# Performance work log

Measured on AMD Instinct MI355X. Metric: run time of the kernel, lower is better.

The kernel has to match this reference:

```python
import jax, jax.numpy as jnp
import numpy as np

B, LQ, LK = 4, 2048, 2048
DQ = DK = DV = DH = 1024


def _xavier(key, shape):
    fan_out, fan_in = shape
    bound = float(np.sqrt(6.0 / (fan_in + fan_out)))
    return jax.random.uniform(key, shape, jnp.float32, -bound, bound)


def setup_inputs() -> dict:
    key = jax.random.key(0)
    ks = jax.random.split(key, 6)
    query = jax.random.normal(ks[0], (B, LQ, DQ), jnp.float32)
    k_in = jax.random.normal(ks[1], (B, LK, DK), jnp.float32)
    key_mask = jax.random.randint(ks[2], (B, LK), 0, 2).astype(bool)
    # torch nn.Linear weights are [out_features, in_features]
    Wk = _xavier(ks[3], (2 * DH, DK))
    bk = jnp.zeros((2 * DH,), jnp.float32)
    Wq = _xavier(ks[4], (DH, DQ))
    bq = jnp.zeros((DH,), jnp.float32)
    Wfc = _xavier(ks[5], (DV, DH))
    bfc = jnp.zeros((DV,), jnp.float32)
    return {"query": query, "key": k_in, "key_mask": key_mask,
            "Wq": Wq, "bq": bq, "Wk": Wk, "bk": bk, "Wfc": Wfc, "bfc": bfc}


def reference(query, key, key_mask, Wq, bq, Wk, bk, Wfc, bfc):
    bs, timesteps, _ = key.shape
    dim = DH
    q = query @ Wq.T + bq                       # [B, Lq, dim]
    c = (key @ Wk.T + bk).reshape(bs, timesteps, 2, dim)
    k = c[:, :, 0]                              # [B, Lk, dim]
    v = c[:, :, 1]                              # [B, Lk, dim]
    scores = jnp.einsum('bqd,bkd->bqk', q, k)   # [B, Lq, Lk]
    scores = jnp.where(key_mask[:, None, :], -jnp.inf, scores)
    attn = jax.nn.softmax(scores, axis=-1)
    out = jnp.einsum('bqk,bkd->bqd', attn, v)   # [B, Lq, dim]
    out = out @ Wfc.T + bfc                     # [B, Lq, DV] (dropout p=0 / eval)
    return out
```

## Files before the change

### kernel.cpp

```cpp
#include <hip/hip_runtime.h>

typedef __attribute__((ext_vector_type(8))) _Float16 half8;
typedef __attribute__((ext_vector_type(4))) _Float16 half4;
typedef __attribute__((ext_vector_type(4))) float f32x4;

__global__ __launch_bounds__(256) void conv4_k(const float4* __restrict__ in,
                                               half4* __restrict__ out){
  int i = blockIdx.x * 256 + threadIdx.x;
  float4 v = in[i];
  half4 h = { (_Float16)v.x, (_Float16)v.y, (_Float16)v.z, (_Float16)v.w };
  out[i] = h;
}

__global__ void mask_detect(const unsigned int* __restrict__ m, int* __restrict__ flag){
  if (threadIdx.x == 0 && blockIdx.x == 0){
    int ok = 1;
#pragma unroll
    for (int j = 0; j < 16; j++){
      unsigned v = m[j];
      if (v != 0u && v != 1u && v != 0x3f800000u) ok = 0;
    }
    *flag = ok;
  }
}

__global__ __launch_bounds__(256) void softmax2048(const float* __restrict__ S,
                                                   _Float16* __restrict__ P){
  const long row = blockIdx.x;
  const float* s = S + row * 2048;
  _Float16* p = P + row * 2048;
  const int tid = threadIdx.x;
  float v[8];
  float m = -1e30f;
#pragma unroll
  for (int i = 0; i < 8; i++){ v[i] = s[tid + i * 256]; m = fmaxf(m, v[i]); }
#pragma unroll
  for (int o = 32; o; o >>= 1) m = fmaxf(m, __shfl_xor(m, o));
  __shared__ float rm[4], rs[4];
  if ((tid & 63) == 0) rm[tid >> 6] = m;
  __syncthreads();
  m = fmaxf(fmaxf(rm[0], rm[1]), fmaxf(rm[2], rm[3]));
  float sum = 0.f;
#pragma unroll
  for (int i = 0; i < 8; i++){ v[i] = __expf(v[i] - m); sum += v[i]; }
#pragma unroll
  for (int o = 32; o; o >>= 1) sum += __shfl_xor(sum, o);
  if ((tid & 63) == 0) rs[tid >> 6] = sum;
  __syncthreads();
  sum = rs[0] + rs[1] + rs[2] + rs[3];
  const float inv = 1.0f / sum;
#pragma unroll
  for (int i = 0; i < 8; i++) p[tid + i * 256] = (_Float16)(v[i] * inv);
}

#define GLL(gp, ldsoff) \
  __builtin_amdgcn_global_load_lds((const __attribute__((address_space(1))) void*)(gp), \
                                   (__attribute__((address_space(3))) void*)&lds[ldsoff], 16, 0, 0)

template<int EPI>
__global__ __launch_bounds__(256)
void gemm_bt(const unsigned short* __restrict__ A, const unsigned short* __restrict__ B,
             int lda, int ldb, int K,
             const float* __restrict__ bias, const void* __restrict__ mask,
             const int* __restrict__ maskFlag,
             void* __restrict__ out0, int ldc,
             long aBS, long bBS, long oBS, int maskBS)
{
  __shared__ short lds[2 * 128 * 32];

  const int z = blockIdx.z;
  const long zA = (long)z * aBS, zB = (long)z * bBS;
  const int tid = threadIdx.x;
  const int lane = tid & 63, wid = tid >> 6;
  const int wr = wid >> 1, wc = wid & 1;
  const int fr = lane & 15, fk = lane >> 4;
  const int brow = blockIdx.x * 128, bcol = blockIdx.y * 128;

  f32x4 acc[4][4];
  const f32x4 fzero = {0.f, 0.f, 0.f, 0.f};
#pragma unroll
  for (int i = 0; i < 4; i++)
#pragma unroll
    for (int j = 0; j < 4; j++) acc[i][j] = fzero;

  const int offA = (wr * 64 + fr) * 32 + fk * 8;
  const int offB = (wc * 64 + fr) * 32 + fk * 8;
  const int srow = tid >> 2;
  const int sck  = (tid & 3) * 8;

  for (int k0 = 0; k0 < K; k0 += 32) {
    __syncthreads();
    {
      const unsigned short* gA = A + zA + (long)(brow + srow) * lda + k0 + sck;
      GLL(gA, tid * 8);
      GLL(gA + (long)64 * lda, (256 + tid) * 8);
      const unsigned short* gB = B + zB + (long)(bcol + srow) * ldb + k0 + sck;
      GLL(gB, 4096 + tid * 8);
      GLL(gB + (long)64 * ldb, 4096 + (256 + tid) * 8);
    }
    __syncthreads();

    half8 a[4], b[4];
#pragma unroll
    for (int i = 0; i < 4; i++){
      a[i] = *(const half8*)&lds[offA + i * 512];
      b[i] = *(const half8*)&lds[4096 + offB + i * 512];
    }
#pragma unroll
    for (int mi = 0; mi < 4; mi++)
#pragma unroll
      for (int ni = 0; ni < 4; ni++)
        acc[mi][ni] = __builtin_amdgcn_mfma_f32_16x16x32_f16(a[mi], b[ni], acc[mi][ni], 0, 0, 0);
  }

  const long zO = (long)z * oBS;
  int mflag = 0;
  if constexpr (EPI == 1) mflag = *maskFlag;
#pragma unroll
  for (int mi = 0; mi < 4; mi++){
#pragma unroll
    for (int ni = 0; ni < 4; ni++){
      const int col = bcol + wc * 64 + ni * 16 + fr;
      float bv = 0.f;
      if constexpr (EPI != 1) { if (bias) bv = bias[col]; }
      bool msk = false;
      if constexpr (EPI == 1) {
        msk = mflag ? (((const int*)mask)[(long)z * maskBS + col] != 0)
                    : (((const unsigned char*)mask)[(long)z * maskBS + col] != 0);
      }
#pragma unroll
      for (int r = 0; r < 4; r++){
        const int row = brow + wr * 64 + mi * 16 + fk * 4 + r;
        float v = acc[mi][ni][r] + bv;
        if constexpr (EPI == 0) {
          ((float*)out0)[zO + (long)row * ldc + col] = v;
        } else if constexpr (EPI == 1) {
          ((float*)out0)[zO + (long)row * ldc + col] = msk ? -1e30f : v;
        } else if constexpr (EPI == 2) {
          ((_Float16*)out0)[zO + (long)row * ldc + col] = (_Float16)v;
        } else {
          const int bb = row >> 11, t = row & 2047;
          ((_Float16*)out0)[(long)bb * 2048 * 1024 + (long)col * 2048 + t] = (_Float16)v;
        }
      }
    }
  }
}

extern "C" void kernel_launch(void* const* d_in, const int* in_sizes, int n_in,
                              void* d_out, int out_size, void* d_ws, size_t ws_size,
                              hipStream_t stream)
{
  (void)in_sizes; (void)n_in; (void)out_size; (void)ws_size;
  const float* query = (const float*)d_in[0];
  const float* key   = (const float*)d_in[1];
  const void*  kmask = d_in[2];
  const float* Wq    = (const float*)d_in[3];
  const float* bq    = (const float*)d_in[4];
  const float* Wk    = (const float*)d_in[5];
  const float* bk    = (const float*)d_in[6];
  const float* Wfc   = (const float*)d_in[7];
  const float* bfc   = (const float*)d_in[8];
  float* out = (float*)d_out;

  char* ws = (char*)d_ws;
  size_t o = 0;
  auto take = [&](size_t bytes)->char*{
    char* p = ws + o;
    o += (bytes + 255) & ~(size_t)255;
    return p;
  };
  const size_t SZ_H = (size_t)8192 * 1024 * 2;

  int* maskFlag           = (int*)take(256);
  unsigned short* query_h = (unsigned short*)take(SZ_H);
  unsigned short* key_h   = (unsigned short*)take(SZ_H);
  unsigned short* Wq_h    = (unsigned short*)take((size_t)1024 * 1024 * 2);
  unsigned short* Wk_h    = (unsigned short*)take((size_t)2048 * 1024 * 2);
  unsigned short* Wfc_h   = (unsigned short*)take((size_t)1024 * 1024 * 2);
  unsigned short* Q       = (unsigned short*)take(SZ_H);
  unsigned short* K       = (unsigned short*)take(SZ_H);
  unsigned short* VT      = (unsigned short*)take(SZ_H);
  unsigned short* O       = (unsigned short*)take(SZ_H);
  float*          S       = (float*)take((size_t)8192 * 2048 * 4);
  unsigned short* P       = (unsigned short*)take((size_t)8192 * 2048 * 2);

  mask_detect<<<1, 64, 0, stream>>>((const unsigned int*)kmask, maskFlag);

  conv4_k<<<8192, 256, 0, stream>>>((const float4*)query, (half4*)query_h);
  conv4_k<<<8192, 256, 0, stream>>>((const float4*)key,   (half4*)key_h);
  conv4_k<<<1024, 256, 0, stream>>>((const float4*)Wq,    (half4*)Wq_h);
  conv4_k<<<2048, 256, 0, stream>>>((const float4*)Wk,    (half4*)Wk_h);
  conv4_k<<<1024, 256, 0, stream>>>((const float4*)Wfc,   (half4*)Wfc_h);

  gemm_bt<2><<<dim3(64, 8, 1), 256, 0, stream>>>(
      query_h, Wq_h, 1024, 1024, 1024,
      bq, nullptr, nullptr, Q, 1024, 0, 0, 0, 0);

  gemm_bt<2><<<dim3(64, 8, 1), 256, 0, stream>>>(
      key_h, Wk_h, 1024, 1024, 1024,
      bk, nullptr, nullptr, K, 1024, 0, 0, 0, 0);

  gemm_bt<4><<<dim3(64, 8, 1), 256, 0, stream>>>(
      key_h, Wk_h + (size_t)1024 * 1024, 1024, 1024, 1024,
      bk + 1024, nullptr, nullptr, VT, 0, 0, 0, 0, 0);

  gemm_bt<1><<<dim3(16, 16, 4), 256, 0, stream>>>(
      Q, K, 1024, 1024, 1024,
      nullptr, kmask, maskFlag, S, 2048,
      (long)2048 * 1024, (long)2048 * 1024, (long)2048 * 2048, 2048);

  softmax2048<<<8192, 256, 0, stream>>>(S, (_Float16*)P);

  gemm_bt<2><<<dim3(16, 8, 4), 256, 0, stream>>>(
      P, VT, 2048, 2048, 2048,
      nullptr, nullptr, nullptr, O, 1024,
      (long)2048 * 2048, (long)1024 * 2048, (long)2048 * 1024, 0);

  gemm_bt<0><<<dim3(64, 8, 1), 256, 0, stream>>>(
      O, Wfc_h, 1024, 1024, 1024,
      bfc, nullptr, nullptr, out, 1024, 0, 0, 0, 0);
}
```

Baseline: 403.2 us.

## Double-buffer LDS tiles in gemm_bt to overlap global loads with MFMA

The GEMM main loop now uses two LDS buffers. It issues the asynchronous global-to-LDS loads for the next K tile before running the MFMAs on the current tile, and needs only one barrier per iteration instead of two. The goal is to hide global memory latency behind matrix-core work in every GEMM stage of the attention pipeline. In exchange, LDS use per block doubles to 32 KB, which may reduce occupancy. Correctness relies on the barrier waiting for the outstanding global_load_lds transfers.

```diff
diff --git a/kernel.cpp b/kernel.cpp
--- a/kernel.cpp
+++ b/kernel.cpp
@@ -66,7 +66,7 @@
              void* __restrict__ out0, int ldc,
              long aBS, long bBS, long oBS, int maskBS)
 {
-  __shared__ short lds[2 * 128 * 32];
+  __shared__ short lds[2 * 8192];
 
   const int z = blockIdx.z;
   const long zA = (long)z * aBS, zB = (long)z * bBS;
@@ -88,30 +88,43 @@
   const int srow = tid >> 2;
   const int sck  = (tid & 3) * 8;
 
-  for (int k0 = 0; k0 < K; k0 += 32) {
-    __syncthreads();
-    {
-      const unsigned short* gA = A + zA + (long)(brow + srow) * lda + k0 + sck;
-      GLL(gA, tid * 8);
-      GLL(gA + (long)64 * lda, (256 + tid) * 8);
-      const unsigned short* gB = B + zB + (long)(bcol + srow) * ldb + k0 + sck;
-      GLL(gB, 4096 + tid * 8);
-      GLL(gB + (long)64 * ldb, 4096 + (256 + tid) * 8);
-    }
-    __syncthreads();
-
+  const unsigned short* gA0 = A + zA + (long)(brow + srow) * lda + sck;
+  const unsigned short* gB0 = B + zB + (long)(bcol + srow) * ldb + sck;
+  const long a64 = (long)64 * lda, b64 = (long)64 * ldb;
+
+#define STAGE(base, k0)                              \
+  do {                                               \
+    GLL(gA0 + (k0),       (base) + tid * 8);         \
+    GLL(gA0 + (k0) + a64, (base) + (256 + tid) * 8); \
+    GLL(gB0 + (k0),       (base) + 4096 + tid * 8);  \
+    GLL(gB0 + (k0) + b64, (base) + 4096 + (256 + tid) * 8); \
+  } while (0)
+
+  const int nt = K >> 5;
+  STAGE(0, 0);
+  __syncthreads();
+
+  int cur = 0;
+  for (int t = 0; t < nt; ++t) {
+    if (t + 1 < nt) STAGE((cur ^ 1) * 8192, (t + 1) << 5);
+
+    const int ab = cur * 8192;
     half8 a[4], b[4];
 #pragma unroll
     for (int i = 0; i < 4; i++){
-      a[i] = *(const half8*)&lds[offA + i * 512];
-      b[i] = *(const half8*)&lds[4096 + offB + i * 512];
+      a[i] = *(const half8*)&lds[ab + offA + i * 512];
+      b[i] = *(const half8*)&lds[ab + 4096 + offB + i * 512];
     }
 #pragma unroll
     for (int mi = 0; mi < 4; mi++)
 #pragma unroll
       for (int ni = 0; ni < 4; ni++)
         acc[mi][ni] = __builtin_amdgcn_mfma_f32_16x16x32_f16(a[mi], b[ni], acc[mi][ni], 0, 0, 0);
+
+    __syncthreads();
+    cur ^= 1;
   }
+#undef STAGE
 
   const long zO = (long)z * oBS;
   int mflag = 0;
```

Result: faster. 362.0 us (-10.2%).

## Replace GEMM with 256-row double-buffered pipelined kernel using 512 threads

Applied to the files above, without the earlier changes.

Replaces the 128x128, 256-thread, single-buffered GEMM with a 256xBN tile (BN=128 or 256), 512-thread kernel. The new kernel double-buffers LDS with a K-step of 64 and splits each iteration into phases so async global-to-LDS loads for the next tile overlap with MFMA work, using raw barriers, vmcnt waits and setprio. The aim is to hide load latency and raise data reuse per LDS byte. The cost is more LDS and registers per block, and fewer blocks on the smaller GEMMs, which lowers grid parallelism.

```diff
diff --git a/kernel.cpp b/kernel.cpp
--- a/kernel.cpp
+++ b/kernel.cpp
@@ -56,71 +56,130 @@
 #define GLL(gp, ldsoff) \
   __builtin_amdgcn_global_load_lds((const __attribute__((address_space(1))) void*)(gp), \
                                    (__attribute__((address_space(3))) void*)&lds[ldsoff], 16, 0, 0)
-
-template<int EPI>
-__global__ __launch_bounds__(256)
-void gemm_bt(const unsigned short* __restrict__ A, const unsigned short* __restrict__ B,
-             int lda, int ldb, int K,
-             const float* __restrict__ bias, const void* __restrict__ mask,
-             const int* __restrict__ maskFlag,
-             void* __restrict__ out0, int ldc,
-             long aBS, long bBS, long oBS, int maskBS)
+#define BAR() asm volatile("s_barrier" ::: "memory")
+#define VMCNT(n) asm volatile("s_waitcnt vmcnt(" #n ")" ::: "memory")
+
+template<int EPI, int NREP>
+__global__ __launch_bounds__(512, 2)
+void gemm256(const unsigned short* __restrict__ A, const unsigned short* __restrict__ B,
+             int lda, int ldb, int K, const float* __restrict__ bias,
+             const void* __restrict__ mask, const int* __restrict__ maskFlag,
+             void* __restrict__ out0, int ldc, long aBS, long bBS, long oBS, int maskBS)
 {
-  __shared__ short lds[2 * 128 * 32];
+  constexpr int BN     = 64 * NREP;
+  constexpr int BUFSZ  = 16384 + 4096 * NREP;
+  constexpr int NCHUNK = 2 + NREP / 2;
+  __shared__ short lds[2 * BUFSZ];
 
   const int z = blockIdx.z;
   const long zA = (long)z * aBS, zB = (long)z * bBS;
   const int tid = threadIdx.x;
   const int lane = tid & 63, wid = tid >> 6;
-  const int wr = wid >> 1, wc = wid & 1;
+  const int wr = wid >> 2, wc = wid & 3;
   const int fr = lane & 15, fk = lane >> 4;
-  const int brow = blockIdx.x * 128, bcol = blockIdx.y * 128;
-
-  f32x4 acc[4][4];
+  const int brow = blockIdx.x * 256, bcol = blockIdx.y * BN;
+
+  f32x4 acc[8][NREP];
   const f32x4 fzero = {0.f, 0.f, 0.f, 0.f};
 #pragma unroll
-  for (int i = 0; i < 4; i++)
-#pragma unroll
-    for (int j = 0; j < 4; j++) acc[i][j] = fzero;
-
-  const int offA = (wr * 64 + fr) * 32 + fk * 8;
-  const int offB = (wc * 64 + fr) * 32 + fk * 8;
-  const int srow = tid >> 2;
-  const int sck  = (tid & 3) * 8;
-
-  for (int k0 = 0; k0 < K; k0 += 32) {
-    __syncthreads();
-    {
-      const unsigned short* gA = A + zA + (long)(brow + srow) * lda + k0 + sck;
-      GLL(gA, tid * 8);
-      GLL(gA + (long)64 * lda, (256 + tid) * 8);
-      const unsigned short* gB = B + zB + (long)(bcol + srow) * ldb + k0 + sck;
-      GLL(gB, 4096 + tid * 8);
-      GLL(gB + (long)64 * ldb, 4096 + (256 + tid) * 8);
-    }
-    __syncthreads();
-
-    half8 a[4], b[4];
-#pragma unroll
-    for (int i = 0; i < 4; i++){
-      a[i] = *(const half8*)&lds[offA + i * 512];
-      b[i] = *(const half8*)&lds[4096 + offB + i * 512];
-    }
-#pragma unroll
-    for (int mi = 0; mi < 4; mi++)
-#pragma unroll
-      for (int ni = 0; ni < 4; ni++)
-        acc[mi][ni] = __builtin_amdgcn_mfma_f32_16x16x32_f16(a[mi], b[ni], acc[mi][ni], 0, 0, 0);
+  for (int i = 0; i < 8; i++)
+#pragma unroll
+    for (int j = 0; j < NREP; j++) acc[i][j] = fzero;
+
+  const int srow = tid >> 3, scol = (tid & 7) * 8;
+  const unsigned short* Ag = A + zA + (long)(brow + srow) * lda + scol;
+  const unsigned short* Bg = B + zB + (long)(bcol + srow) * ldb + scol;
+  const int aoff = (wr * 128 + fr) * 64 + fk * 8;
+  const int boff = (wc * 16 * NREP + fr) * 64 + fk * 8;
+
+  auto stage = [&](int nb, int c, long k1) {
+    if (c < 2) {
+      const unsigned short* g = Ag + (long)(c * 128) * lda + k1;
+      GLL(g,                  nb + c * 8192 + tid * 8);
+      GLL(g + (long)64 * lda, nb + c * 8192 + 4096 + tid * 8);
+    } else {
+      const unsigned short* g = Bg + (long)((c - 2) * 128) * ldb + k1;
+      GLL(g,                  nb + 16384 + (c - 2) * 8192 + tid * 8);
+      GLL(g + (long)64 * ldb, nb + 16384 + (c - 2) * 8192 + 4096 + tid * 8);
+    }
+  };
+
+  half8 a[4][2], b[NREP][2];
+  auto readA = [&](int cb, int qm) {
+#pragma unroll
+    for (int mi = 0; mi < 4; ++mi)
+#pragma unroll
+      for (int kk = 0; kk < 2; ++kk)
+        a[mi][kk] = *(const half8*)&lds[cb + aoff + qm * 4096 + mi * 1024 + kk * 32];
+  };
+  auto readB = [&](int cb, int n0, int n1) {
+#pragma unroll
+    for (int ni = n0; ni < n1; ++ni)
+#pragma unroll
+      for (int kk = 0; kk < 2; ++kk)
+        b[ni][kk] = *(const half8*)&lds[cb + 16384 + boff + ni * 1024 + kk * 32];
+  };
+  auto mmaQ = [&](int qm, int n0, int n1) {
+#pragma unroll
+    for (int mi = 0; mi < 4; ++mi)
+#pragma unroll
+      for (int ni = n0; ni < n1; ++ni) {
+        f32x4 c = acc[qm * 4 + mi][ni];
+        c = __builtin_amdgcn_mfma_f32_16x16x32_f16(a[mi][0], b[ni][0], c, 0, 0, 0);
+        c = __builtin_amdgcn_mfma_f32_16x16x32_f16(a[mi][1], b[ni][1], c, 0, 0, 0);
+        acc[qm * 4 + mi][ni] = c;
+      }
+  };
+
+  const int nt = K >> 6;
+  for (int c = 0; c < NCHUNK; ++c) stage(0, c, 0);
+
+  for (int t = 0; t < nt; ++t) {
+    const int cb = (t & 1) ? BUFSZ : 0, nb = cb ^ BUFSZ;
+    const long k1 = (long)(t + 1) << 6;
+    const bool pf = (t + 1 < nt);
+    if constexpr (NREP == 4) {
+      if (pf) { stage(nb, 0, k1); VMCNT(2); } else VMCNT(0);
+      BAR();
+      readA(cb, 0); readB(cb, 0, 2);
+      __builtin_amdgcn_s_setprio(1); mmaQ(0, 0, 2); __builtin_amdgcn_s_setprio(0);
+      BAR();
+      if (pf) stage(nb, 1, k1);
+      readB(cb, 2, 4);
+      BAR();
+      __builtin_amdgcn_s_setprio(1); mmaQ(0, 2, 4); __builtin_amdgcn_s_setprio(0);
+      BAR();
+      if (pf) stage(nb, 2, k1);
+      readA(cb, 1);
+      BAR();
+      __builtin_amdgcn_s_setprio(1); mmaQ(1, 2, 4); __builtin_amdgcn_s_setprio(0);
+      BAR();
+      if (pf) stage(nb, 3, k1);
+      BAR();
+      __builtin_amdgcn_s_setprio(1); mmaQ(1, 0, 2); __builtin_amdgcn_s_setprio(0);
+      BAR();
+    } else {
+      if (pf) { stage(nb, 0, k1); stage(nb, 1, k1); VMCNT(4); } else VMCNT(0);
+      BAR();
+      readA(cb, 0); readB(cb, 0, 2);
+      __builtin_amdgcn_s_setprio(1); mmaQ(0, 0, 2); __builtin_amdgcn_s_setprio(0);
+      BAR();
+      if (pf) stage(nb, 2, k1);
+      readA(cb, 1);
+      BAR();
+      __builtin_amdgcn_s_setprio(1); mmaQ(1, 0, 2); __builtin_amdgcn_s_setprio(0);
+      BAR();
+    }
   }
 
   const long zO = (long)z * oBS;
   int mflag = 0;
   if constexpr (EPI == 1) mflag = *maskFlag;
 #pragma unroll
-  for (int mi = 0; mi < 4; mi++){
-#pragma unroll
-    for (int ni = 0; ni < 4; ni++){
-      const int col = bcol + wc * 64 + ni * 16 + fr;
+  for (int mi = 0; mi < 8; ++mi) {
+#pragma unroll
+    for (int ni = 0; ni < NREP; ++ni) {
+      const int col = bcol + wc * 16 * NREP + ni * 16 + fr;
       float bv = 0.f;
       if constexpr (EPI != 1) { if (bias) bv = bias[col]; }
       bool msk = false;
@@ -129,8 +188,8 @@
                     : (((const unsigned char*)mask)[(long)z * maskBS + col] != 0);
       }
 #pragma unroll
-      for (int r = 0; r < 4; r++){
-        const int row = brow + wr * 64 + mi * 16 + fk * 4 + r;
+      for (int r = 0; r < 4; ++r) {
+        const int row = brow + wr * 128 + mi * 16 + fk * 4 + r;
         float v = acc[mi][ni][r] + bv;
         if constexpr (EPI == 0) {
           ((float*)out0)[zO + (long)row * ldc + col] = v;
@@ -139,8 +198,8 @@
         } else if constexpr (EPI == 2) {
           ((_Float16*)out0)[zO + (long)row * ldc + col] = (_Float16)v;
         } else {
-          const int bb = row >> 11, t = row & 2047;
-          ((_Float16*)out0)[(long)bb * 2048 * 1024 + (long)col * 2048 + t] = (_Float16)v;
+          const int bb = row >> 11, tt = row & 2047;
+          ((_Float16*)out0)[(long)bb * 2048 * 1024 + (long)col * 2048 + tt] = (_Float16)v;
         }
       }
     }
@@ -193,31 +252,31 @@
   conv4_k<<<2048, 256, 0, stream>>>((const float4*)Wk,    (half4*)Wk_h);
   conv4_k<<<1024, 256, 0, stream>>>((const float4*)Wfc,   (half4*)Wfc_h);
 
-  gemm_bt<2><<<dim3(64, 8, 1), 256, 0, stream>>>(
+  gemm256<2, 2><<<dim3(32, 8, 1), 512, 0, stream>>>(
       query_h, Wq_h, 1024, 1024, 1024,
       bq, nullptr, nullptr, Q, 1024, 0, 0, 0, 0);
 
-  gemm_bt<2><<<dim3(64, 8, 1), 256, 0, stream>>>(
+  gemm256<2, 2><<<dim3(32, 8, 1), 512, 0, stream>>>(
       key_h, Wk_h, 1024, 1024, 1024,
       bk, nullptr, nullptr, K, 1024, 0, 0, 0, 0);
 
-  gemm_bt<4><<<dim3(64, 8, 1), 256, 0, stream>>>(
+  gemm256<4, 2><<<dim3(32, 8, 1), 512, 0, stream>>>(
       key_h, Wk_h + (size_t)1024 * 1024, 1024, 1024, 1024,
       bk + 1024, nullptr, nullptr, VT, 0, 0, 0, 0, 0);
 
-  gemm_bt<1><<<dim3(16, 16, 4), 256, 0, stream>>>(
+  gemm256<1, 4><<<dim3(8, 8, 4), 512, 0, stream>>>(
       Q, K, 1024, 1024, 1024,
       nullptr, kmask, maskFlag, S, 2048,
       (long)2048 * 1024, (long)2048 * 1024, (long)2048 * 2048, 2048);
 
   softmax2048<<<8192, 256, 0, stream>>>(S, (_Float16*)P);
 
-  gemm_bt<2><<<dim3(16, 8, 4), 256, 0, stream>>>(
+  gemm256<2, 2><<<dim3(8, 8, 4), 512, 0, stream>>>(
       P, VT, 2048, 2048, 2048,
       nullptr, nullptr, nullptr, O, 1024,
       (long)2048 * 2048, (long)1024 * 2048, (long)2048 * 1024, 0);
 
-  gemm_bt<0><<<dim3(64, 8, 1), 256, 0, stream>>>(
+  gemm256<0, 2><<<dim3(32, 8, 1), 512, 0, stream>>>(
       O, Wfc_h, 1024, 1024, 1024,
       bfc, nullptr, nullptr, out, 1024, 0, 0, 0, 0);
 }
```

New measurement: 406.1 us. Within noise of the previous version (+0.7%).
